# Kernel optimization log

Hardware: AMD Instinct MI355X
Metric: run time of the kernel (lower is better)

The kernel has to match this reference:

```python
import jax, jax.numpy as jnp
import numpy as np

N_NODES = 50000
N_EDGES = 800000
N_SUPPORTS = 2
D_IN = 512
D_OUT = 128


def setup_inputs() -> dict:
    key = jax.random.key(0)
    ks = jax.random.split(key, 6)
    x = jax.random.normal(ks[0], (N_NODES, D_IN), dtype=jnp.float32)
    kernels = jax.random.normal(ks[1], (N_SUPPORTS, D_IN, D_OUT), dtype=jnp.float32) * 0.05
    bias = jax.random.normal(ks[2], (D_OUT,), dtype=jnp.float32) * 0.05
    adj_vals = jax.random.uniform(ks[3], (N_SUPPORTS, N_EDGES), dtype=jnp.float32)
    adj_rows = jax.random.randint(ks[4], (N_SUPPORTS, N_EDGES), 0, N_NODES, dtype=jnp.int32)
    adj_cols = jax.random.randint(ks[5], (N_SUPPORTS, N_EDGES), 0, N_NODES, dtype=jnp.int32)
    return {"x": x, "kernels": kernels, "bias": bias,
            "adj_vals": adj_vals, "adj_rows": adj_rows, "adj_cols": adj_cols}


def _spmm(vals, rows, cols, dense):
    # COO sparse [N,N] @ dense [N,F] -> [N,F]
    gathered = vals[:, None] * dense[cols]            # [E, F]
    return jax.ops.segment_sum(gathered, rows, num_segments=N_NODES)


def reference(x, kernels, bias, adj_vals, adj_rows, adj_cols):
    # dropout rate = 0.0 -> identity
    out = jnp.zeros((N_NODES, D_OUT), dtype=x.dtype)
    for s in range(N_SUPPORTS):  # small fixed number of supports
        pre_sup = x @ kernels[s]                      # [N, D_OUT]
        out = out + _spmm(adj_vals[s], adj_rows[s], adj_cols[s], pre_sup)
    out = out + bias
    return jax.nn.relu(out)
```

## Files before the change

kernel.cpp:

```cpp
#include <hip/hip_runtime.h>

#define N_NODES 50000
#define N_EDGES 800000
#define D_IN    512
#define D_OUT   128
#define N_SUP   2
#define N_COLS  (N_SUP * D_OUT)
#define BINS    (N_SUP * N_NODES)
#define NB_S    196
#define NB      (N_SUP * NB_S)
#define CAP     4608
#define CHUNK   4096
#define NCHUNK  ((N_EDGES + CHUNK - 1) / CHUNK)

typedef __attribute__((ext_vector_type(8))) __bf16 bf16x8;
typedef __attribute__((ext_vector_type(4))) float  f32x4;

__global__ __launch_bounds__(256) void convert_w(const float* __restrict__ w,
                                                 __bf16* __restrict__ wt2,
                                                 int* __restrict__ gcursor) {
    const int g = blockIdx.x * 256 + threadIdx.x;
    if (g < NB) gcursor[g] = 0;
    if (g >= (D_IN / 8) * N_COLS) return;
    const int kq = g >> 8;
    const int n  = g & 255;
    const int s  = n >> 7;
    const int np = n & 127;
    bf16x8 v;
#pragma unroll
    for (int j = 0; j < 8; ++j) {
        const int k = kq * 8 + j;
        v[j] = (__bf16)w[((size_t)s * D_IN + k) * D_OUT + np];
    }
    *(bf16x8*)(wt2 + (size_t)g * 8) = v;
}

__global__ __launch_bounds__(256) void gemm_bf16(const float* __restrict__ x,
                                                 const __bf16* __restrict__ wt2,
                                                 __bf16* __restrict__ pre) {
    __shared__ __align__(16) __bf16 Bs[2048 * 8];

    const int t    = threadIdx.x;
    const int lane = t & 63;
    const int w    = t >> 6;
    const int l15  = lane & 15;
    const int quad = lane >> 4;

    const int rbase = blockIdx.x * 64 + w * 16;
    int arow = rbase + l15;
    if (arow >= N_NODES) arow = N_NODES - 1;
    const float* aptr = x + (size_t)arow * D_IN + quad * 8;

    f32x4 acc[16];
#pragma unroll
    for (int i = 0; i < 16; ++i) acc[i] = (f32x4)0.f;

    for (int kb = 0; kb < 8; ++kb) {
        const __bf16* gsrc = wt2 + ((size_t)kb * 2048 + w * 64 + lane) * 8;
#pragma unroll
        for (int i = 0; i < 8; ++i) {
            __builtin_amdgcn_global_load_lds(
                (const __attribute__((address_space(1))) unsigned int*)(gsrc + (size_t)i * 2048),
                (__attribute__((address_space(3))) unsigned int*)(&Bs[(i * 256 + w * 64) * 8]),
                16, 0, 0);
        }
        bf16x8 afrag[2];
#pragma unroll
        for (int kk = 0; kk < 2; ++kk) {
            const float* ap = aptr + kb * 64 + kk * 32;
            float4 f0 = *(const float4*)(ap);
            float4 f1 = *(const float4*)(ap + 4);
            bf16x8 a;
            a[0] = (__bf16)f0.x; a[1] = (__bf16)f0.y;
            a[2] = (__bf16)f0.z; a[3] = (__bf16)f0.w;
            a[4] = (__bf16)f1.x; a[5] = (__bf16)f1.y;
            a[6] = (__bf16)f1.z; a[7] = (__bf16)f1.w;
            afrag[kk] = a;
        }
        __syncthreads();

#pragma unroll
        for (int kk = 0; kk < 2; ++kk) {
            const __bf16* bbase = &Bs[((kk * 4 + quad) * 256 + l15) * 8];
#pragma unroll
            for (int ct = 0; ct < 16; ++ct) {
                bf16x8 b = *(const bf16x8*)(bbase + ct * 128);
                acc[ct] = __builtin_amdgcn_mfma_f32_16x16x32_bf16(afrag[kk], b, acc[ct], 0, 0, 0);
            }
        }
        __syncthreads();
    }

#pragma unroll
    for (int ct = 0; ct < 16; ++ct) {
        const int col = ct * 16 + l15;
        const int s   = col >> 7;
        const int cp  = col & 127;
#pragma unroll
        for (int r = 0; r < 4; ++r) {
            const int row = rbase + quad * 4 + r;
            if (row < N_NODES)
                pre[((size_t)s * N_NODES + row) * D_OUT + cp] = (__bf16)acc[ct][r];
        }
    }
}

__global__ __launch_bounds__(256) void scatter_coarse(const float* __restrict__ adj_vals,
                                                      const int* __restrict__ adj_rows,
                                                      const int* __restrict__ adj_cols,
                                                      int* __restrict__ gcursor,
                                                      uint2* __restrict__ coarse) {
    __shared__ int hist[NB_S];
    __shared__ int excl[NB_S];
    __shared__ int lbase[NB_S];
    __shared__ int rankc[NB_S];
    __shared__ int sc[256];
    __shared__ uint2 buf[CHUNK];

    const int s = blockIdx.y;
    const int t = threadIdx.x;
    if (t < NB_S) { hist[t] = 0; rankc[t] = 0; }
    __syncthreads();

    const int e0 = blockIdx.x * CHUNK;
    int   rr[16]; int cc[16]; float vv[16];
#pragma unroll
    for (int i = 0; i < 16; ++i) {
        const int e = e0 + i * 256 + t;
        if (e < N_EDGES) {
            const size_t src = (size_t)s * N_EDGES + e;
            rr[i] = adj_rows[src];
            cc[i] = adj_cols[src];
            vv[i] = adj_vals[src];
            atomicAdd(&hist[rr[i] >> 8], 1);
        } else {
            rr[i] = -1; cc[i] = 0; vv[i] = 0.f;
        }
    }
    __syncthreads();

    sc[t] = (t < NB_S) ? hist[t] : 0;
    __syncthreads();
    for (int off = 1; off < 256; off <<= 1) {
        const int a = (t >= off) ? sc[t - off] : 0;
        __syncthreads();
        sc[t] += a;
        __syncthreads();
    }
    if (t < NB_S) {
        excl[t]  = sc[t] - hist[t];
        lbase[t] = hist[t] ? atomicAdd(&gcursor[s * NB_S + t], hist[t]) : 0;
    }
    __syncthreads();

#pragma unroll
    for (int i = 0; i < 16; ++i) {
        if (rr[i] >= 0) {
            const int b   = rr[i] >> 8;
            const int pos = excl[b] + atomicAdd(&rankc[b], 1);
            buf[pos] = make_uint2(__float_as_uint(vv[i]),
                                  ((unsigned)rr[i] << 16) | (unsigned)cc[i]);
        }
    }
    __syncthreads();

    const int total = min(e0 + CHUNK, N_EDGES) - e0;
    for (int i = t; i < total; i += 256) {
        const uint2 ed = buf[i];
        const int b   = ed.y >> 24;
        const int dst = lbase[b] + (i - excl[b]);
        if (dst < CAP)
            coarse[(size_t)(s * NB_S + b) * CAP + dst] = ed;
    }
}

__global__ __launch_bounds__(256) void scatter_fine(const uint2* __restrict__ coarse,
                                                    const int* __restrict__ gcursor,
                                                    uint2* __restrict__ sorted,
                                                    int* __restrict__ row_off,
                                                    int* __restrict__ row_cnt) {
    __shared__ int rh[256];
    __shared__ int sd[256];
    __shared__ int rex[256];
    __shared__ int rc[256];
    __shared__ uint2 buf[CAP];

    const int bk = blockIdx.x;
    const int s  = blockIdx.y;
    const int t  = threadIdx.x;
    const int bkt = s * NB_S + bk;
    const size_t b0 = (size_t)bkt * CAP;
    const int cnt = min(gcursor[bkt], CAP);

    rh[t] = 0; rc[t] = 0;
    __syncthreads();

    uint2 ev[18];
#pragma unroll
    for (int j = 0; j < 18; ++j) {
        const int i = j * 256 + t;
        if (i < cnt) {
            ev[j] = coarse[b0 + i];
            atomicAdd(&rh[(ev[j].y >> 16) & 255], 1);
        }
    }
    __syncthreads();

    const int myc = rh[t];
    sd[t] = myc;
    __syncthreads();
    for (int off = 1; off < 256; off <<= 1) {
        const int a = (t >= off) ? sd[t - off] : 0;
        __syncthreads();
        sd[t] += a;
        __syncthreads();
    }
    const int ex = sd[t] - myc;
    rex[t] = ex;
    const int row = (bk << 8) + t;
    if (row < N_NODES) {
        row_off[s * N_NODES + row] = (int)(b0 + ex);
        row_cnt[s * N_NODES + row] = myc;
    }
    __syncthreads();

#pragma unroll
    for (int j = 0; j < 18; ++j) {
        const int i = j * 256 + t;
        if (i < cnt) {
            const int rl   = (ev[j].y >> 16) & 255;
            const int pos  = rex[rl] + atomicAdd(&rc[rl], 1);
            buf[pos] = make_uint2(ev[j].x, ev[j].y & 0xFFFFu);
        }
    }
    __syncthreads();

    for (int i = t; i < cnt; i += 256)
        sorted[b0 + i] = buf[i];
}

__global__ __launch_bounds__(256) void gather_spmm(const int* __restrict__ row_off,
                                                   const int* __restrict__ row_cnt,
                                                   const uint2* __restrict__ sorted,
                                                   const uint4* __restrict__ pre_q,
                                                   const float* __restrict__ bias,
                                                   float* __restrict__ out) {
    const int lane = threadIdx.x & 63;
    const int q    = lane >> 4;
    const int fl   = lane & 15;
    const int row  = blockIdx.x * 4 + (threadIdx.x >> 6);
    if (row >= N_NODES) return;

    float a[8];
#pragma unroll
    for (int k = 0; k < 8; ++k) a[k] = 0.f;

#pragma unroll
    for (int s = 0; s < N_SUP; ++s) {
        const int bin   = s * N_NODES + row;
        const int start = row_off[bin];
        const int cnt   = row_cnt[bin];
        const uint4* psup = pre_q + (size_t)s * N_NODES * 16 + fl;

        for (int e0 = 0; e0 < cnt; e0 += 64) {
            const int m = min(64, cnt - e0);
            int   c = 0;
            float v = 0.f;
            if (lane < m) {
                const uint2 ed = sorted[start + e0 + lane];
                v = __uint_as_float(ed.x);
                c = (int)ed.y;
            }
            const int steps = (m + 3) >> 2;

            auto step = [&](int jj) {
                const int   idx = (jj < m) ? jj : 0;
                float vj = __shfl(v, idx);
                const int cj = __shfl(c, idx);
                if (jj >= m) vj = 0.f;
                const uint4 p = psup[(size_t)cj * 16];
                a[0] += vj * __uint_as_float(p.x << 16);
                a[1] += vj * __uint_as_float(p.x & 0xffff0000u);
                a[2] += vj * __uint_as_float(p.y << 16);
                a[3] += vj * __uint_as_float(p.y & 0xffff0000u);
                a[4] += vj * __uint_as_float(p.z << 16);
                a[5] += vj * __uint_as_float(p.z & 0xffff0000u);
                a[6] += vj * __uint_as_float(p.w << 16);
                a[7] += vj * __uint_as_float(p.w & 0xffff0000u);
            };
            int jj = 0;
            for (; jj + 1 < steps; jj += 2) {
                step(jj * 4 + q);
                step(jj * 4 + 4 + q);
            }
            if (jj < steps) step(jj * 4 + q);
        }
    }

#pragma unroll
    for (int k = 0; k < 8; ++k) {
        a[k] += __shfl_xor(a[k], 16);
        a[k] += __shfl_xor(a[k], 32);
    }

    if (lane < 16) {
        const float4 b0 = *(const float4*)(bias + fl * 8);
        const float4 b1 = *(const float4*)(bias + fl * 8 + 4);
        float4 o0, o1;
        o0.x = fmaxf(a[0] + b0.x, 0.f);
        o0.y = fmaxf(a[1] + b0.y, 0.f);
        o0.z = fmaxf(a[2] + b0.z, 0.f);
        o0.w = fmaxf(a[3] + b0.w, 0.f);
        o1.x = fmaxf(a[4] + b1.x, 0.f);
        o1.y = fmaxf(a[5] + b1.y, 0.f);
        o1.z = fmaxf(a[6] + b1.z, 0.f);
        o1.w = fmaxf(a[7] + b1.w, 0.f);
        float* dst = out + (size_t)row * D_OUT + fl * 8;
        *(float4*)(dst)     = o0;
        *(float4*)(dst + 4) = o1;
    }
}

extern "C" void kernel_launch(void* const* d_in, const int* in_sizes, int n_in,
                              void* d_out, int out_size, void* d_ws, size_t ws_size,
                              hipStream_t stream) {
    const float* x        = (const float*)d_in[0];
    const float* kernels  = (const float*)d_in[1];
    const float* bias     = (const float*)d_in[2];
    const float* adj_vals = (const float*)d_in[3];
    const int*   adj_rows = (const int*)d_in[4];
    const int*   adj_cols = (const int*)d_in[5];
    float* out = (float*)d_out;

    char* ws = (char*)d_ws;
    size_t off = 0;
    auto alloc = [&](size_t bytes) {
        char* p = ws + off;
        off += (bytes + 255) & ~(size_t)255;
        return p;
    };
    __bf16* pre    = (__bf16*)alloc(sizeof(__bf16) * N_SUP * N_NODES * D_OUT);
    __bf16* wt2    = (__bf16*)alloc(sizeof(__bf16) * D_IN * N_COLS);
    uint2*  coarse = (uint2*) alloc(sizeof(uint2)  * NB * CAP);
    uint2*  sorted = (uint2*) alloc(sizeof(uint2)  * NB * CAP);
    int*    row_off = (int*)alloc(sizeof(int) * BINS);
    int*    row_cnt = (int*)alloc(sizeof(int) * BINS);
    int*    gcursor = (int*)alloc(sizeof(int) * NB);

    convert_w<<<(D_IN / 8) * N_COLS / 256, 256, 0, stream>>>(kernels, wt2, gcursor);
    gemm_bf16<<<(N_NODES + 63) / 64, 256, 0, stream>>>(x, wt2, pre);

    dim3 gc(NCHUNK, N_SUP);
    scatter_coarse<<<gc, 256, 0, stream>>>(adj_vals, adj_rows, adj_cols, gcursor, coarse);
    dim3 gf(NB_S, N_SUP);
    scatter_fine<<<gf, 256, 0, stream>>>(coarse, gcursor, sorted, row_off, row_cnt);

    gather_spmm<<<(N_NODES + 3) / 4, 256, 0, stream>>>(row_off, row_cnt, sorted,
                                                       (const uint4*)pre, bias, out);
}
```

Measured before the change: 276.5 us.

## Co-schedule GEMM halves with sparse scatter passes in fused launches

Splits the dense GEMM row blocks into two halves. Each half runs in the same launch as one of the two sorting passes (coarse and fine bucket scatter), with the role picked by block index. The goal is to overlap the compute-bound GEMM with the memory- and atomic-bound scatter work and to remove one kernel launch. The cost is a shared-memory footprint sized to the largest role, which may lower occupancy, and possible load imbalance between the two kinds of block.

```diff
diff --git a/kernel.cpp b/kernel.cpp
--- a/kernel.cpp
+++ b/kernel.cpp
@@ -12,6 +12,8 @@
 #define CAP     4608
 #define CHUNK   4096
 #define NCHUNK  ((N_EDGES + CHUNK - 1) / CHUNK)
+#define GEMM_BLOCKS ((N_NODES + 63) / 64)
+#define GHALF   391
 
 typedef __attribute__((ext_vector_type(8))) __bf16 bf16x8;
 typedef __attribute__((ext_vector_type(4))) float  f32x4;
@@ -35,10 +37,10 @@
     *(bf16x8*)(wt2 + (size_t)g * 8) = v;
 }
 
-__global__ __launch_bounds__(256) void gemm_bf16(const float* __restrict__ x,
-                                                 const __bf16* __restrict__ wt2,
-                                                 __bf16* __restrict__ pre) {
-    __shared__ __align__(16) __bf16 Bs[2048 * 8];
+__device__ __forceinline__ void gemm_body(int rowblk, const float* __restrict__ x,
+                                          const __bf16* __restrict__ wt2,
+                                          __bf16* __restrict__ pre, char* smem) {
+    __bf16* Bs = (__bf16*)smem;
 
     const int t    = threadIdx.x;
     const int lane = t & 63;
@@ -46,7 +48,7 @@
     const int l15  = lane & 15;
     const int quad = lane >> 4;
 
-    const int rbase = blockIdx.x * 64 + w * 16;
+    const int rbase = rowblk * 64 + w * 16;
     int arow = rbase + l15;
     if (arow >= N_NODES) arow = N_NODES - 1;
     const float* aptr = x + (size_t)arow * D_IN + quad * 8;
@@ -105,24 +107,25 @@
     }
 }
 
-__global__ __launch_bounds__(256) void scatter_coarse(const float* __restrict__ adj_vals,
-                                                      const int* __restrict__ adj_rows,
-                                                      const int* __restrict__ adj_cols,
-                                                      int* __restrict__ gcursor,
-                                                      uint2* __restrict__ coarse) {
-    __shared__ int hist[NB_S];
-    __shared__ int excl[NB_S];
-    __shared__ int lbase[NB_S];
-    __shared__ int rankc[NB_S];
-    __shared__ int sc[256];
-    __shared__ uint2 buf[CHUNK];
-
-    const int s = blockIdx.y;
+__device__ __forceinline__ void coarse_body(int cid,
+                                            const float* __restrict__ adj_vals,
+                                            const int* __restrict__ adj_rows,
+                                            const int* __restrict__ adj_cols,
+                                            int* __restrict__ gcursor,
+                                            uint2* __restrict__ coarse, char* smem) {
+    int*   hist  = (int*)smem;
+    int*   excl  = hist + NB_S;
+    int*   lbase = excl + NB_S;
+    int*   rankc = lbase + NB_S;
+    int*   sc    = rankc + NB_S;
+    uint2* buf   = (uint2*)(smem + 4160);
+
+    const int s = cid / NCHUNK;
     const int t = threadIdx.x;
     if (t < NB_S) { hist[t] = 0; rankc[t] = 0; }
     __syncthreads();
 
-    const int e0 = blockIdx.x * CHUNK;
+    const int e0 = (cid % NCHUNK) * CHUNK;
     int   rr[16]; int cc[16]; float vv[16];
 #pragma unroll
     for (int i = 0; i < 16; ++i) {
@@ -174,19 +177,20 @@
     }
 }
 
-__global__ __launch_bounds__(256) void scatter_fine(const uint2* __restrict__ coarse,
-                                                    const int* __restrict__ gcursor,
-                                                    uint2* __restrict__ sorted,
-                                                    int* __restrict__ row_off,
-                                                    int* __restrict__ row_cnt) {
-    __shared__ int rh[256];
-    __shared__ int sd[256];
-    __shared__ int rex[256];
-    __shared__ int rc[256];
-    __shared__ uint2 buf[CAP];
-
-    const int bk = blockIdx.x;
-    const int s  = blockIdx.y;
+__device__ __forceinline__ void fine_body(int fid,
+                                          const uint2* __restrict__ coarse,
+                                          const int* __restrict__ gcursor,
+                                          uint2* __restrict__ sorted,
+                                          int* __restrict__ row_off,
+                                          int* __restrict__ row_cnt, char* smem) {
+    int*   rh  = (int*)smem;
+    int*   sd  = rh + 256;
+    int*   rex = sd + 256;
+    int*   rc  = rex + 256;
+    uint2* buf = (uint2*)(smem + 4096);
+
+    const int s  = fid / NB_S;
+    const int bk = fid % NB_S;
     const int t  = threadIdx.x;
     const int bkt = s * NB_S + bk;
     const size_t b0 = (size_t)bkt * CAP;
@@ -237,6 +241,38 @@
 
     for (int i = t; i < cnt; i += 256)
         sorted[b0 + i] = buf[i];
+}
+
+__global__ __launch_bounds__(256) void fused_gemm_coarse(const float* __restrict__ x,
+                                                         const __bf16* __restrict__ wt2,
+                                                         __bf16* __restrict__ pre,
+                                                         const float* __restrict__ adj_vals,
+                                                         const int* __restrict__ adj_rows,
+                                                         const int* __restrict__ adj_cols,
+                                                         int* __restrict__ gcursor,
+                                                         uint2* __restrict__ coarse) {
+    __shared__ __align__(16) char smem[36928];
+    const int bid = blockIdx.x;
+    if (bid < GHALF)
+        gemm_body(bid, x, wt2, pre, smem);
+    else
+        coarse_body(bid - GHALF, adj_vals, adj_rows, adj_cols, gcursor, coarse, smem);
+}
+
+__global__ __launch_bounds__(256) void fused_gemm_fine(const float* __restrict__ x,
+                                                       const __bf16* __restrict__ wt2,
+                                                       __bf16* __restrict__ pre,
+                                                       const uint2* __restrict__ coarse,
+                                                       const int* __restrict__ gcursor,
+                                                       uint2* __restrict__ sorted,
+                                                       int* __restrict__ row_off,
+                                                       int* __restrict__ row_cnt) {
+    __shared__ __align__(16) char smem[40960];
+    const int bid = blockIdx.x;
+    if (bid < GEMM_BLOCKS - GHALF)
+        gemm_body(GHALF + bid, x, wt2, pre, smem);
+    else
+        fine_body(bid - (GEMM_BLOCKS - GHALF), coarse, gcursor, sorted, row_off, row_cnt, smem);
 }
 
 __global__ __launch_bounds__(256) void gather_spmm(const int* __restrict__ row_off,
@@ -348,12 +384,14 @@
     int*    gcursor = (int*)alloc(sizeof(int) * NB);
 
     convert_w<<<(D_IN / 8) * N_COLS / 256, 256, 0, stream>>>(kernels, wt2, gcursor);
-    gemm_bf16<<<(N_NODES + 63) / 64, 256, 0, stream>>>(x, wt2, pre);
-
-    dim3 gc(NCHUNK, N_SUP);
-    scatter_coarse<<<gc, 256, 0, stream>>>(adj_vals, adj_rows, adj_cols, gcursor, coarse);
-    dim3 gf(NB_S, N_SUP);
-    scatter_fine<<<gf, 256, 0, stream>>>(coarse, gcursor, sorted, row_off, row_cnt);
+
+    fused_gemm_coarse<<<GHALF + NB, 256, 0, stream>>>(x, wt2, pre,
+                                                      adj_vals, adj_rows, adj_cols,
+                                                      gcursor, coarse);
+
+    fused_gemm_fine<<<(GEMM_BLOCKS - GHALF) + NB, 256, 0, stream>>>(x, wt2, pre,
+                                                                    coarse, gcursor, sorted,
+                                                                    row_off, row_cnt);
 
     gather_spmm<<<(N_NODES + 3) / 4, 256, 0, stream>>>(row_off, row_cnt, sorted,
                                                        (const uint4*)pre, bias, out);
```

New measurement: 271.0 us. 1.02x faster.

## Rewrite GEMM as persistent kernel with register-resident weights and swizzled A tiles

Applied to the files above, without the earlier changes.

The dense x@W GEMM becomes a persistent kernel of 256 blocks with 512 threads. Each wave keeps its slice of the bf16 weight matrix in registers for the whole run. Blocks walk 16-row tiles of x, staging each tile through XOR-swizzled LDS and prefetching the next tile into registers while the MFMAs run. This drops the per-block reloading of the whole weight matrix through LDS, at the cost of heavy register use (32 bf16x8 fragments per lane) and small tiles with two barriers per tile.

```diff
diff --git a/kernel.cpp b/kernel.cpp
--- a/kernel.cpp
+++ b/kernel.cpp
@@ -13,6 +13,10 @@
 #define CHUNK   4096
 #define NCHUNK  ((N_EDGES + CHUNK - 1) / CHUNK)
 
+#define TILE_R  16
+#define NTILES  (N_NODES / TILE_R)
+#define GGRID   256
+
 typedef __attribute__((ext_vector_type(8))) __bf16 bf16x8;
 typedef __attribute__((ext_vector_type(4))) float  f32x4;
 
@@ -35,10 +39,10 @@
     *(bf16x8*)(wt2 + (size_t)g * 8) = v;
 }
 
-__global__ __launch_bounds__(256) void gemm_bf16(const float* __restrict__ x,
-                                                 const __bf16* __restrict__ wt2,
-                                                 __bf16* __restrict__ pre) {
-    __shared__ __align__(16) __bf16 Bs[2048 * 8];
+__global__ __launch_bounds__(512, 2) void gemm_bf16_v2(const float* __restrict__ x,
+                                                       const __bf16* __restrict__ wt2,
+                                                       __bf16* __restrict__ pre) {
+    __shared__ __align__(16) __bf16 As[TILE_R * 64 * 8];
 
     const int t    = threadIdx.x;
     const int lane = t & 63;
@@ -46,62 +50,69 @@
     const int l15  = lane & 15;
     const int quad = lane >> 4;
 
-    const int rbase = blockIdx.x * 64 + w * 16;
-    int arow = rbase + l15;
-    if (arow >= N_NODES) arow = N_NODES - 1;
-    const float* aptr = x + (size_t)arow * D_IN + quad * 8;
-
-    f32x4 acc[16];
-#pragma unroll
-    for (int i = 0; i < 16; ++i) acc[i] = (f32x4)0.f;
-
-    for (int kb = 0; kb < 8; ++kb) {
-        const __bf16* gsrc = wt2 + ((size_t)kb * 2048 + w * 64 + lane) * 8;
-#pragma unroll
-        for (int i = 0; i < 8; ++i) {
-            __builtin_amdgcn_global_load_lds(
-                (const __attribute__((address_space(1))) unsigned int*)(gsrc + (size_t)i * 2048),
-                (__attribute__((address_space(3))) unsigned int*)(&Bs[(i * 256 + w * 64) * 8]),
-                16, 0, 0);
-        }
-        bf16x8 afrag[2];
-#pragma unroll
-        for (int kk = 0; kk < 2; ++kk) {
-            const float* ap = aptr + kb * 64 + kk * 32;
-            float4 f0 = *(const float4*)(ap);
-            float4 f1 = *(const float4*)(ap + 4);
-            bf16x8 a;
-            a[0] = (__bf16)f0.x; a[1] = (__bf16)f0.y;
-            a[2] = (__bf16)f0.z; a[3] = (__bf16)f0.w;
-            a[4] = (__bf16)f1.x; a[5] = (__bf16)f1.y;
-            a[6] = (__bf16)f1.z; a[7] = (__bf16)f1.w;
-            afrag[kk] = a;
-        }
-        __syncthreads();
-
-#pragma unroll
-        for (int kk = 0; kk < 2; ++kk) {
-            const __bf16* bbase = &Bs[((kk * 4 + quad) * 256 + l15) * 8];
-#pragma unroll
-            for (int ct = 0; ct < 16; ++ct) {
-                bf16x8 b = *(const bf16x8*)(bbase + ct * 128);
-                acc[ct] = __builtin_amdgcn_mfma_f32_16x16x32_bf16(afrag[kk], b, acc[ct], 0, 0, 0);
-            }
-        }
-        __syncthreads();
-    }
-
-#pragma unroll
-    for (int ct = 0; ct < 16; ++ct) {
-        const int col = ct * 16 + l15;
-        const int s   = col >> 7;
-        const int cp  = col & 127;
+    bf16x8 B0[16], B1[16];
+#pragma unroll
+    for (int kb = 0; kb < 16; ++kb) {
+        const size_t g0 = (size_t)(kb * 4 + quad) * 256 + w * 32 + l15;
+        B0[kb] = *(const bf16x8*)(wt2 + g0 * 8);
+        B1[kb] = *(const bf16x8*)(wt2 + (g0 + 16) * 8);
+    }
+
+    const int s_out = w >> 2;
+    const int cp0   = (w & 3) * 32 + l15;
+
+    const int srow = t >> 5;
+    const int sc0  = (t & 31) * 2;
+    const int swz  = srow & 7;
+
+    int tile = blockIdx.x;
+    float4 f0, f1, f2, f3;
+    {
+        const float* src = x + ((size_t)tile * TILE_R + srow) * D_IN + sc0 * 8;
+        f0 = ((const float4*)src)[0];
+        f1 = ((const float4*)src)[1];
+        f2 = ((const float4*)src)[2];
+        f3 = ((const float4*)src)[3];
+    }
+
+    while (tile < NTILES) {
+        bf16x8 lo, hi;
+        lo[0] = (__bf16)f0.x; lo[1] = (__bf16)f0.y; lo[2] = (__bf16)f0.z; lo[3] = (__bf16)f0.w;
+        lo[4] = (__bf16)f1.x; lo[5] = (__bf16)f1.y; lo[6] = (__bf16)f1.z; lo[7] = (__bf16)f1.w;
+        hi[0] = (__bf16)f2.x; hi[1] = (__bf16)f2.y; hi[2] = (__bf16)f2.z; hi[3] = (__bf16)f2.w;
+        hi[4] = (__bf16)f3.x; hi[5] = (__bf16)f3.y; hi[6] = (__bf16)f3.z; hi[7] = (__bf16)f3.w;
+
+        __syncthreads();
+        *(bf16x8*)&As[((size_t)srow * 64 + (sc0       ^ swz)) * 8] = lo;
+        *(bf16x8*)&As[((size_t)srow * 64 + ((sc0 + 1) ^ swz)) * 8] = hi;
+        __syncthreads();
+
+        const int next = tile + GGRID;
+        if (next < NTILES) {
+            const float* src = x + ((size_t)next * TILE_R + srow) * D_IN + sc0 * 8;
+            f0 = ((const float4*)src)[0];
+            f1 = ((const float4*)src)[1];
+            f2 = ((const float4*)src)[2];
+            f3 = ((const float4*)src)[3];
+        }
+
+        f32x4 acc0 = (f32x4)0.f, acc1 = (f32x4)0.f;
+#pragma unroll
+        for (int kb = 0; kb < 16; ++kb) {
+            const int c = (kb * 4 + quad) ^ (l15 & 7);
+            bf16x8 a = *(const bf16x8*)&As[((size_t)l15 * 64 + c) * 8];
+            acc0 = __builtin_amdgcn_mfma_f32_16x16x32_bf16(a, B0[kb], acc0, 0, 0, 0);
+            acc1 = __builtin_amdgcn_mfma_f32_16x16x32_bf16(a, B1[kb], acc1, 0, 0, 0);
+        }
+
+        __bf16* dst = pre + ((size_t)s_out * N_NODES + (size_t)tile * TILE_R + quad * 4) * D_OUT + cp0;
 #pragma unroll
         for (int r = 0; r < 4; ++r) {
-            const int row = rbase + quad * 4 + r;
-            if (row < N_NODES)
-                pre[((size_t)s * N_NODES + row) * D_OUT + cp] = (__bf16)acc[ct][r];
-        }
+            dst[(size_t)r * D_OUT]      = (__bf16)acc0[r];
+            dst[(size_t)r * D_OUT + 16] = (__bf16)acc1[r];
+        }
+
+        tile = next;
     }
 }
 
@@ -348,7 +359,8 @@
     int*    gcursor = (int*)alloc(sizeof(int) * NB);
 
     convert_w<<<(D_IN / 8) * N_COLS / 256, 256, 0, stream>>>(kernels, wt2, gcursor);
-    gemm_bf16<<<(N_NODES + 63) / 64, 256, 0, stream>>>(x, wt2, pre);
+
+    gemm_bf16_v2<<<GGRID, 512, 0, stream>>>(x, wt2, pre);
 
     dim3 gc(NCHUNK, N_SUP);
     scatter_coarse<<<gc, 256, 0, stream>>>(adj_vals, adj_rows, adj_cols, gcursor, coarse);
```

New measurement: 266.0 us. -3.8%, faster.
